# Optimization experiments

Hardware: AMD Instinct MI355X
Metric: run time of the kernel (lower is better)

Reference implementation:

```python
import jax, jax.numpy as jnp
import numpy as np

B, N, P, D = 16, 358, 72, 96
ND, H, K = 64, 4, 10
HL = H // 2
HG = H - HL
NH = 4  # temporal attention heads


def ln(x, g, b, eps=1e-5):
    m = x.mean(-1, keepdims=True)
    v = ((x - m) ** 2).mean(-1, keepdims=True)
    return (x - m) / jnp.sqrt(v + eps) * g + b


def topk_sparsify(adj, k):
    # row-wise top-k masking + renormalization, vectorized over all leading dims
    shp = adj.shape
    n = shp[-1]
    flat = adj.reshape(-1, shp[-2], n)
    M, R = flat.shape[0], flat.shape[1]
    _, idx = jax.lax.top_k(flat, k)  # (M,R,k)
    mask = jnp.zeros(flat.shape, flat.dtype).at[
        jnp.arange(M)[:, None, None], jnp.arange(R)[None, :, None], idx].set(1.0)
    sp = flat * mask
    sp = sp / (sp.sum(-1, keepdims=True) + 1e-8)
    return sp.reshape(shp)


def forward(patch_features, local_e1, local_e2, global_e1, global_e2, static_e2,
            temperature, pos_enc, wq, bq, wk, bk, wv, bv, wo, bo, tn_g, tn_b,
            de_w1, de_b1, de_g1, de_beta1, de_w2, de_b2, de_g2, de_beta2,
            gnn_w, gnn_b, gnn_g, gnn_beta, gf_w, gf_b,
            ee_w1, ee_b1, ee_g, ee_beta, ee_w2, ee_b2, ee_w3, ee_b3):
    # ---- static multi-head graphs (batched over heads instead of python loop) ----
    adj_l = jax.nn.relu(jnp.einsum('hnd,hdm->hnm', local_e1, local_e2))
    t_l = jnp.clip(temperature[:HL] * 2.0, 0.1, 5.0)
    adj_l = jax.nn.softmax(adj_l / t_l[:, None, None], axis=-1)
    adj_g = jax.nn.relu(jnp.einsum('hnd,hdm->hnm', global_e1, global_e2))
    t_g = jnp.clip(temperature[HL:] * 0.5, 0.1, 2.0)
    adj_g = jax.nn.softmax(adj_g / t_g[:, None, None], axis=-1)
    static_adjs = jnp.concatenate([adj_l, adj_g], axis=0)  # (H,N,N)

    # ---- dynamic graphs ----
    b, n, p, d = patch_features.shape
    pr = patch_features.reshape(b * n, p, d)
    x = pr + pos_enc[:, :p]
    hd = d // NH
    q = (x @ wq + bq).reshape(-1, p, NH, hd).transpose(0, 2, 1, 3)
    kk = (x @ wk + bk).reshape(-1, p, NH, hd).transpose(0, 2, 1, 3)
    v = (x @ wv + bv).reshape(-1, p, NH, hd).transpose(0, 2, 1, 3)
    att = jax.nn.softmax(jnp.einsum('bhqd,bhkd->bhqk', q, kk) / np.float32(np.sqrt(hd)), axis=-1)
    o = jnp.einsum('bhqk,bhkd->bhqd', att, v).transpose(0, 2, 1, 3).reshape(-1, p, d)
    attended = o @ wo + bo  # (BN,P,D)
    imp = jax.nn.softmax(attended.mean(-1), axis=1)  # (BN,P)
    node = (attended * imp[..., None]).sum(1) + pr.mean(1)
    node = ln(node, tn_g, tn_b).reshape(b, n, d)
    h1 = jax.nn.gelu(ln(node @ de_w1 + de_b1, de_g1, de_beta1), approximate=False)
    dyn = ln(h1 @ de_w2 + de_b2, de_g2, de_beta2)  # (B,N,ND)
    for i in range(2):  # 2 structurally distinct GNN layers, batched over B
        sim = jax.nn.softmax(jnp.einsum('bnd,bmd->bnm', dyn, dyn) / 0.2, axis=-1)
        agg = jnp.einsum('bnm,bmd->bnd', sim, dyn)
        out = jax.nn.gelu(ln(agg @ gnn_w[i] + gnn_b[i], gnn_g[i], gnn_beta[i]), approximate=False)
        dyn = out + dyn
    dsim = jax.nn.relu(jnp.einsum('bnd,hdm->bhnm', dyn, static_e2))
    t_d = jnp.clip(temperature, 0.1, 2.0)
    dynamic_adjs = jax.nn.softmax(dsim / t_d[None, :, None, None], axis=-1)  # (B,H,N,N)

    static_adjs = topk_sparsify(static_adjs, K)
    dynamic_adjs = topk_sparsify(dynamic_adjs, K)

    # ---- static/dynamic fusion ----
    node_f = patch_features.mean(2)  # (B,N,D)
    fw = jax.nn.sigmoid(node_f @ gf_w + gf_b)  # (B,N,H)
    w = jnp.transpose(fw, (0, 2, 1))[..., None]  # (B,H,N,1), broadcast over columns
    fused = (1.0 - w) * static_adjs[None] + w * dynamic_adjs  # (B,H,N,N)

    # ---- edge encoder over head dim ----
    mh = jnp.transpose(fused, (0, 2, 3, 1))  # (B,N,N,H)
    e = jax.nn.gelu(ln(mh @ ee_w1 + ee_b1, ee_g, ee_beta), approximate=False)
    e = jax.nn.gelu(e @ ee_w2 + ee_b2, approximate=False)
    e = (e @ ee_w3 + ee_b3)[..., 0]  # (B,N,N)
    final = jax.nn.sigmoid(e) * fused.mean(1)
    return final, static_adjs, dynamic_adjs


def setup_inputs() -> dict:
    key = jax.random.key(0)
    ks = jax.random.split(key, 20)
    r = lambda i, shape, s=0.05: jax.random.normal(ks[i], shape, dtype=jnp.float32) * s
    z = lambda shape: jnp.zeros(shape, jnp.float32)
    o = lambda shape: jnp.ones(shape, jnp.float32)
    return dict(
        patch_features=r(0, (B, N, P, D), 1.0),
        local_e1=r(1, (HL, N, ND // 2), 0.1),
        local_e2=r(2, (HL, ND // 2, N), 0.1),
        global_e1=r(3, (HG, N, ND), 0.1),
        global_e2=r(4, (HG, ND, N), 0.1),
        static_e2=r(5, (H, ND, N), 0.1),
        temperature=jnp.full((H,), 0.5, jnp.float32),
        pos_enc=r(6, (1, 72, D), 0.02),
        wq=r(7, (D, D)), bq=z((D,)),
        wk=r(8, (D, D)), bk=z((D,)),
        wv=r(9, (D, D)), bv=z((D,)),
        wo=r(10, (D, D)), bo=z((D,)),
        tn_g=o((D,)), tn_b=z((D,)),
        de_w1=r(11, (D, 2 * ND)), de_b1=z((2 * ND,)),
        de_g1=o((2 * ND,)), de_beta1=z((2 * ND,)),
        de_w2=r(12, (2 * ND, ND)), de_b2=z((ND,)),
        de_g2=o((ND,)), de_beta2=z((ND,)),
        gnn_w=r(13, (2, ND, ND)), gnn_b=z((2, ND)),
        gnn_g=o((2, ND)), gnn_beta=z((2, ND)),
        gf_w=r(14, (D, H)), gf_b=z((H,)),
        ee_w1=r(15, (H, 4 * H)), ee_b1=z((4 * H,)),
        ee_g=o((4 * H,)), ee_beta=z((4 * H,)),
        ee_w2=r(16, (4 * H, 2 * H)), ee_b2=z((2 * H,)),
        ee_w3=r(17, (2 * H, 1)), ee_b3=z((1,)),
    )


def reference(patch_features, local_e1, local_e2, global_e1, global_e2, static_e2,
              temperature, pos_enc, wq, bq, wk, bk, wv, bv, wo, bo, tn_g, tn_b,
              de_w1, de_b1, de_g1, de_beta1, de_w2, de_b2, de_g2, de_beta2,
              gnn_w, gnn_b, gnn_g, gnn_beta, gf_w, gf_b,
              ee_w1, ee_b1, ee_g, ee_beta, ee_w2, ee_b2, ee_w3, ee_b3):
    return forward(patch_features, local_e1, local_e2, global_e1, global_e2, static_e2,
                   temperature, pos_enc, wq, bq, wk, bk, wv, bv, wo, bo, tn_g, tn_b,
                   de_w1, de_b1, de_g1, de_beta1, de_w2, de_b2, de_g2, de_beta2,
                   gnn_w, gnn_b, gnn_g, gnn_beta, gf_w, gf_b,
                   ee_w1, ee_b1, ee_g, ee_beta, ee_w2, ee_b2, ee_w3, ee_b3)
```

## Files before the change

### kernel.cpp

```cpp
#include <hip/hip_runtime.h>
#include <hip/hip_bf16.h>

#define B_ 16
#define N_ 358
#define P_ 72
#define D_ 96
#define ND_ 64
#define H_ 4
#define NH_ 4
#define HD_ 24
#define K_ 10
#define BN_ (B_*N_)
#define NN_ (N_*N_)
#define RPW_ 6

__device__ __forceinline__ float gelu_f(float x){ return 0.5f*x*(1.0f+erff(x*0.7071067811865476f)); }
__device__ __forceinline__ float sigm_f(float x){ return 1.0f/(1.0f+expf(-x)); }

__global__ __launch_bounds__(256) void attn_kernel(
    const float* __restrict__ patch, const float* __restrict__ pos,
    const float* __restrict__ wq, const float* __restrict__ bq,
    const float* __restrict__ wk, const float* __restrict__ bk,
    const float* __restrict__ wv, const float* __restrict__ bv,
    const float* __restrict__ wo, const float* __restrict__ bo,
    const float* __restrict__ tng, const float* __restrict__ tnb,
    float* __restrict__ node_out, float* __restrict__ meanpr_out)
{
    __shared__ float smem[10656];
    __shared__ float rr[P_];
    __shared__ float nb[D_];
    __shared__ float st2[2];

    float* const xs  = smem;
    float* const qh  = smem;
    float* const kh  = smem + 1800;
    float* const vh  = smem + 3600;
    float* const att = smem + 5400;
    float* const ats = smem;

    const int tid = threadIdx.x;
    const int tc  = tid & 31;
    const int tr  = tid >> 5;
    const int rbase = tr * 9;
    const int bn  = blockIdx.x;
    const float* pr = patch + (size_t)bn * (P_*D_);

    float mpr = 0.f;
    if (tid < D_) {
        for (int p = 0; p < P_; ++p) mpr += pr[p*D_+tid];
        mpr *= (1.0f/P_);
        meanpr_out[(size_t)bn*D_ + tid] = mpr;
    }

    for (int e = tid; e < P_*D_; e += 256) {
        int row = e / D_, col = e - row*D_;
        xs[row*97 + col] = pr[e] + pos[e];
    }
    __syncthreads();

    float aq[3][9], ak[3][9], av[3][9];
    #pragma unroll
    for (int j = 0; j < 3; ++j) {
        const int c = tc + 32*j;
        const float vbq = bq[c], vbk = bk[c], vbv = bv[c];
        #pragma unroll
        for (int i = 0; i < 9; ++i) { aq[j][i]=vbq; ak[j][i]=vbk; av[j][i]=vbv; }
    }
    for (int k = 0; k < D_; ++k) {
        float xv[9];
        #pragma unroll
        for (int i = 0; i < 9; ++i) xv[i] = xs[(rbase+i)*97 + k];
        const float* wqp = wq + k*D_;
        const float* wkp = wk + k*D_;
        const float* wvp = wv + k*D_;
        float wqv[3], wkv[3], wvv[3];
        #pragma unroll
        for (int j = 0; j < 3; ++j) {
            const int c = tc + 32*j;
            wqv[j]=wqp[c]; wkv[j]=wkp[c]; wvv[j]=wvp[c];
        }
        #pragma unroll
        for (int j = 0; j < 3; ++j)
            #pragma unroll
            for (int i = 0; i < 9; ++i) {
                aq[j][i] += xv[i]*wqv[j];
                ak[j][i] += xv[i]*wkv[j];
                av[j][i] += xv[i]*wvv[j];
            }
    }
    __syncthreads();

    float ao[3][9];
    #pragma unroll
    for (int j = 0; j < 3; ++j) {
        const float vbo = bo[tc + 32*j];
        #pragma unroll
        for (int i = 0; i < 9; ++i) ao[j][i] = vbo;
    }

    const float rs = 0.20412414523193154f;
    for (int h = 0; h < NH_; ++h) {
        #pragma unroll
        for (int j = 0; j < 3; ++j) {
            const int c = tc + 32*j;
            const int dl = c - HD_*h;
            if ((unsigned)dl < (unsigned)HD_) {
                #pragma unroll
                for (int i = 0; i < 9; ++i) {
                    qh[(rbase+i)*25 + dl] = aq[j][i];
                    kh[(rbase+i)*25 + dl] = ak[j][i];
                    vh[(rbase+i)*25 + dl] = av[j][i];
                }
            }
        }
        __syncthreads();

        {
            float sc[3][9];
            #pragma unroll
            for (int jj = 0; jj < 3; ++jj)
                #pragma unroll
                for (int i = 0; i < 9; ++i) sc[jj][i] = 0.f;
            for (int d = 0; d < HD_; ++d) {
                float qv[9];
                #pragma unroll
                for (int i = 0; i < 9; ++i) qv[i] = qh[(rbase+i)*25 + d];
                float kv[3];
                #pragma unroll
                for (int jj = 0; jj < 3; ++jj) {
                    const int jn = tc + 32*jj;
                    kv[jj] = (jn < P_) ? kh[jn*25 + d] : 0.f;
                }
                #pragma unroll
                for (int jj = 0; jj < 3; ++jj)
                    #pragma unroll
                    for (int i = 0; i < 9; ++i) sc[jj][i] += qv[i]*kv[jj];
            }
            #pragma unroll
            for (int jj = 0; jj < 3; ++jj) {
                const int jn = tc + 32*jj;
                if (jn < P_) {
                    #pragma unroll
                    for (int i = 0; i < 9; ++i)
                        att[(rbase+i)*73 + jn] = sc[jj][i]*rs;
                }
            }
        }
        __syncthreads();

        if (tid < P_) {
            float* ar = att + tid*73;
            float mx = ar[0];
            for (int j = 1; j < P_; ++j) mx = fmaxf(mx, ar[j]);
            float sm = 0.f;
            for (int j = 0; j < P_; ++j) { float ev = expf(ar[j]-mx); ar[j]=ev; sm += ev; }
            float inv = 1.0f/sm;
            for (int j = 0; j < P_; ++j) ar[j] *= inv;
        }
        __syncthreads();

        if (tc < HD_) {
            float ov[9];
            #pragma unroll
            for (int i = 0; i < 9; ++i) ov[i] = 0.f;
            for (int j = 0; j < P_; ++j) {
                const float vv = vh[j*25 + tc];
                #pragma unroll
                for (int i = 0; i < 9; ++i) ov[i] += att[(rbase+i)*73 + j]*vv;
            }
            #pragma unroll
            for (int i = 0; i < 9; ++i) kh[(rbase+i)*25 + tc] = ov[i];
        }
        __syncthreads();

        for (int d = 0; d < HD_; ++d) {
            float ovv[9];
            #pragma unroll
            for (int i = 0; i < 9; ++i) ovv[i] = kh[(rbase+i)*25 + d];
            const float* wop = wo + (HD_*h + d)*D_;
            float wv3[3];
            #pragma unroll
            for (int j = 0; j < 3; ++j) wv3[j] = wop[tc + 32*j];
            #pragma unroll
            for (int j = 0; j < 3; ++j)
                #pragma unroll
                for (int i = 0; i < 9; ++i) ao[j][i] += ovv[i]*wv3[j];
        }
        __syncthreads();
    }

    #pragma unroll
    for (int j = 0; j < 3; ++j) {
        const int c = tc + 32*j;
        #pragma unroll
        for (int i = 0; i < 9; ++i) ats[(rbase+i)*97 + c] = ao[j][i];
    }
    __syncthreads();

    if (tid < P_) {
        const float* ar = ats + tid*97;
        float s = 0.f;
        for (int d = 0; d < D_; ++d) s += ar[d];
        rr[tid] = s*(1.0f/D_);
    }
    __syncthreads();
    if (tid == 0) {
        float mx = rr[0];
        for (int i=1;i<P_;++i) mx = fmaxf(mx, rr[i]);
        float sm=0.f;
        for (int i=0;i<P_;++i){ float ev=expf(rr[i]-mx); rr[i]=ev; sm+=ev; }
        float inv=1.0f/sm;
        for (int i=0;i<P_;++i) rr[i]*=inv;
    }
    __syncthreads();
    if (tid < D_) {
        float s = 0.f;
        for (int i=0;i<P_;++i) s += ats[i*97+tid]*rr[i];
        nb[tid] = s + mpr;
    }
    __syncthreads();
    if (tid == 0) {
        float m=0.f; for(int d=0;d<D_;++d) m+=nb[d]; m *= (1.0f/D_);
        float v=0.f; for(int d=0;d<D_;++d){ float df=nb[d]-m; v+=df*df; } v *= (1.0f/D_);
        st2[0]=m; st2[1]=rsqrtf(v+1e-5f);
    }
    __syncthreads();
    if (tid < D_) {
        float y = (nb[tid]-st2[0])*st2[1]*tng[tid] + tnb[tid];
        node_out[(size_t)bn*D_+tid] = y;
    }
}

__global__ __launch_bounds__(128) void enc1_kernel(
    const float* __restrict__ node, const float* __restrict__ w1, const float* __restrict__ b1,
    const float* __restrict__ g1, const float* __restrict__ be1, float* __restrict__ h1)
{
    __shared__ float nr[D_];
    __shared__ float buf[128];
    __shared__ float st2[2];
    const int tid = threadIdx.x; const int bn = blockIdx.x;
    if (tid < D_) nr[tid] = node[(size_t)bn*D_+tid];
    __syncthreads();
    float s = b1[tid];
    for (int c = 0; c < D_; ++c) s += nr[c]*w1[c*128+tid];
    buf[tid] = s;
    __syncthreads();
    if (tid == 0) {
        float m=0.f; for(int d=0;d<128;++d) m+=buf[d]; m *= (1.0f/128.0f);
        float v=0.f; for(int d=0;d<128;++d){ float df=buf[d]-m; v+=df*df; } v *= (1.0f/128.0f);
        st2[0]=m; st2[1]=rsqrtf(v+1e-5f);
    }
    __syncthreads();
    float y = (buf[tid]-st2[0])*st2[1]*g1[tid] + be1[tid];
    h1[(size_t)bn*128+tid] = gelu_f(y);
}

__global__ __launch_bounds__(64) void enc2_kernel(
    const float* __restrict__ h1, const float* __restrict__ w2, const float* __restrict__ b2,
    const float* __restrict__ g2, const float* __restrict__ be2, float* __restrict__ dyn)
{
    __shared__ float hr[128];
    __shared__ float buf[ND_];
    __shared__ float st2[2];
    const int tid = threadIdx.x; const int bn = blockIdx.x;
    hr[tid] = h1[(size_t)bn*128+tid];
    hr[tid+64] = h1[(size_t)bn*128+64+tid];
    __syncthreads();
    float s = b2[tid];
    for (int c = 0; c < 128; ++c) s += hr[c]*w2[c*ND_+tid];
    buf[tid] = s;
    __syncthreads();
    if (tid == 0) {
        float m=0.f; for(int d=0;d<ND_;++d) m+=buf[d]; m *= (1.0f/ND_);
        float v=0.f; for(int d=0;d<ND_;++d){ float df=buf[d]-m; v+=df*df; } v *= (1.0f/ND_);
        st2[0]=m; st2[1]=rsqrtf(v+1e-5f);
    }
    __syncthreads();
    dyn[(size_t)bn*ND_+tid] = (buf[tid]-st2[0])*st2[1]*g2[tid] + be2[tid];
}

__global__ __launch_bounds__(256) void gnn_kernel(
    const float* __restrict__ din, float* __restrict__ dout,
    const float* __restrict__ gw, const float* __restrict__ gb,
    const float* __restrict__ gg, const float* __restrict__ gbe, int layer)
{
    __shared__ float dq[ND_];
    __shared__ float prob[N_];
    __shared__ float red[256];
    __shared__ float aggp[4*ND_];
    __shared__ float buf[ND_];
    __shared__ float st2[2];
    const int tid = threadIdx.x; const int bn = blockIdx.x;
    const int b = bn / N_;
    const float* base = din + (size_t)b*N_*ND_;
    if (tid < ND_) dq[tid] = din[(size_t)bn*ND_+tid];
    __syncthreads();

    float lmax = -1e30f;
    for (int m = tid; m < N_; m += 256) {
        const float* rm = base + (size_t)m*ND_;
        float s = 0.f;
        for (int c = 0; c < ND_; ++c) s += dq[c]*rm[c];
        s *= 5.0f;
        prob[m] = s;
        lmax = fmaxf(lmax, s);
    }
    red[tid]=lmax; __syncthreads();
    for (int st=128; st>0; st>>=1){ if(tid<st) red[tid]=fmaxf(red[tid],red[tid+st]); __syncthreads(); }
    const float mx = red[0]; __syncthreads();
    float lsum = 0.f;
    for (int m=tid; m<N_; m+=256){ float ev=expf(prob[m]-mx); prob[m]=ev; lsum+=ev; }
    red[tid]=lsum; __syncthreads();
    for (int st=128; st>0; st>>=1){ if(tid<st) red[tid]+=red[tid+st]; __syncthreads(); }
    const float inv = 1.0f/red[0]; __syncthreads();
    for (int m=tid; m<N_; m+=256) prob[m]*=inv;
    __syncthreads();

    {
        const int part = tid >> 6, d = tid & 63;
        float s = 0.f;
        for (int m = part; m < N_; m += 4) s += prob[m]*base[(size_t)m*ND_+d];
        aggp[part*ND_+d] = s;
    }
    __syncthreads();
    if (tid < ND_)
        aggp[tid] = aggp[tid]+aggp[ND_+tid]+aggp[2*ND_+tid]+aggp[3*ND_+tid];
    __syncthreads();
    if (tid < ND_) {
        float t = gb[layer*ND_+tid];
        for (int c = 0; c < ND_; ++c) t += aggp[c]*gw[(layer*ND_+c)*ND_+tid];
        buf[tid] = t;
    }
    __syncthreads();
    if (tid == 0) {
        float m=0.f; for(int d=0;d<ND_;++d) m+=buf[d]; m *= (1.0f/ND_);
        float v=0.f; for(int d=0;d<ND_;++d){ float df=buf[d]-m; v+=df*df; } v *= (1.0f/ND_);
        st2[0]=m; st2[1]=rsqrtf(v+1e-5f);
    }
    __syncthreads();
    if (tid < ND_) {
        float y = (buf[tid]-st2[0])*st2[1]*gg[layer*ND_+tid] + gbe[layer*ND_+tid];
        dout[(size_t)bn*ND_+tid] = gelu_f(y) + dq[tid];
    }
}

__device__ __forceinline__ void wave_softmax_topk_store(
    float lv[RPW_], int lane, float* __restrict__ outrow)
{
    float mx = 0.f;
    #pragma unroll
    for (int j=0;j<RPW_;++j) mx = fmaxf(mx, lv[j]);
    #pragma unroll
    for (int s=1;s<64;s<<=1) mx = fmaxf(mx, __shfl_xor(mx, s));
    float sm = 0.f;
    #pragma unroll
    for (int j=0;j<RPW_;++j) {
        const int m = lane + 64*j;
        const float e = (m < N_) ? expf(lv[j]-mx) : 0.f;
        lv[j] = e; sm += e;
    }
    #pragma unroll
    for (int s=1;s<64;s<<=1) sm += __shfl_xor(sm, s);
    const float inv = 1.0f/sm;
    #pragma unroll
    for (int j=0;j<RPW_;++j) lv[j] *= inv;

    unsigned sel = 0u;
    float ksum = 0.f;
    for (int it = 0; it < K_; ++it) {
        float bv = -1.f; int bm = 0x7fffffff;
        #pragma unroll
        for (int j=0;j<RPW_;++j) {
            const int m = lane + 64*j;
            if (m < N_ && !((sel>>j)&1u) && lv[j] > bv) { bv = lv[j]; bm = m; }
        }
        #pragma unroll
        for (int s=1;s<64;s<<=1) {
            const float ov = __shfl_xor(bv, s);
            const int   om = __shfl_xor(bm, s);
            if (ov > bv || (ov == bv && om < bm)) { bv = ov; bm = om; }
        }
        ksum += bv;
        if ((bm & 63) == lane) sel |= 1u << (bm >> 6);
    }
    const float dn = 1.0f/(ksum + 1e-8f);
    #pragma unroll
    for (int j=0;j<RPW_;++j) {
        const int m = lane + 64*j;
        if (m < N_) outrow[m] = ((sel>>j)&1u) ? lv[j]*dn : 0.f;
    }
}

__global__ __launch_bounds__(256) void static_adj_kernel(
    const float* __restrict__ le1, const float* __restrict__ le2,
    const float* __restrict__ ge1, const float* __restrict__ ge2,
    const float* __restrict__ temp, float* __restrict__ outs)
{
    __shared__ float e1l[4][ND_];
    const int tid = threadIdx.x;
    const int wv = tid >> 6, lane = tid & 63;
    const int r = blockIdx.x*4 + wv;
    const int h = r / N_, n = r % N_;
    if (h < 2) { if (lane < 32) e1l[wv][lane] = le1[(h*N_+n)*32+lane]; }
    else       { e1l[wv][lane] = ge1[((h-2)*N_+n)*64+lane]; }
    __syncthreads();
    const float t = temp[h];
    const float tl = (h < 2) ? fminf(fmaxf(t*2.0f,0.1f),5.0f) : fminf(fmaxf(t*0.5f,0.1f),2.0f);
    const float invt = 1.0f/tl;
    float lv[RPW_];
    #pragma unroll
    for (int j=0;j<RPW_;++j) lv[j] = 0.f;
    if (h < 2) {
        for (int c = 0; c < 32; ++c) {
            const float dc = e1l[wv][c];
            const float* sr = le2 + (size_t)(h*32+c)*N_;
            #pragma unroll
            for (int j=0;j<RPW_;++j) {
                const int m = lane + 64*j;
                if (m < N_) lv[j] += dc*sr[m];
            }
        }
    } else {
        for (int c = 0; c < 64; ++c) {
            const float dc = e1l[wv][c];
            const float* sr = ge2 + (size_t)((h-2)*64+c)*N_;
            #pragma unroll
            for (int j=0;j<RPW_;++j) {
                const int m = lane + 64*j;
                if (m < N_) lv[j] += dc*sr[m];
            }
        }
    }
    #pragma unroll
    for (int j=0;j<RPW_;++j) lv[j] = fmaxf(lv[j],0.f)*invt;
    wave_softmax_topk_store(lv, lane, outs + (size_t)r*N_);
}

__global__ __launch_bounds__(256) void dyn_adj_kernel(
    const float* __restrict__ dyn, const float* __restrict__ se2,
    const float* __restrict__ temp, float* __restrict__ outd)
{
    __shared__ float dql[4][ND_];
    const int tid = threadIdx.x;
    const int wv = tid >> 6, lane = tid & 63;
    const int r = blockIdx.x*4 + wv;
    const int b = r / (H_*N_);
    const int rem = r % (H_*N_);
    const int h = rem / N_, n = rem % N_;
    dql[wv][lane] = dyn[((size_t)(b*N_+n))*ND_ + lane];
    __syncthreads();
    const float invt = 1.0f/fminf(fmaxf(temp[h],0.1f),2.0f);
    float lv[RPW_];
    #pragma unroll
    for (int j=0;j<RPW_;++j) lv[j] = 0.f;
    const float* sb = se2 + (size_t)h*ND_*N_;
    for (int c = 0; c < ND_; ++c) {
        const float dc = dql[wv][c];
        const float* sr = sb + (size_t)c*N_;
        #pragma unroll
        for (int j=0;j<RPW_;++j) {
            const int m = lane + 64*j;
            if (m < N_) lv[j] += dc*sr[m];
        }
    }
    #pragma unroll
    for (int j=0;j<RPW_;++j) lv[j] = fmaxf(lv[j],0.f)*invt;
    wave_softmax_topk_store(lv, lane, outd + ((size_t)(b*H_+h)*N_+n)*(size_t)N_);
}

__global__ __launch_bounds__(256) void fw_kernel(
    const float* __restrict__ meanpr, const float* __restrict__ gfw,
    const float* __restrict__ gfb, float* __restrict__ wf)
{
    const int gid = blockIdx.x*256 + threadIdx.x;
    if (gid >= BN_*H_) return;
    const int bn = gid >> 2, h = gid & 3;
    float s = gfb[h];
    const float* mp = meanpr + (size_t)bn*D_;
    for (int c=0;c<D_;++c) s += mp[c]*gfw[c*H_+h];
    wf[gid] = sigm_f(s);
}

__global__ __launch_bounds__(256) void edge_kernel(
    const float* __restrict__ staticf, const float* __restrict__ dynf,
    const float* __restrict__ wf,
    const float* __restrict__ ew1, const float* __restrict__ eb1,
    const float* __restrict__ eg,  const float* __restrict__ ebe,
    const float* __restrict__ ew2, const float* __restrict__ eb2,
    const float* __restrict__ ew3, const float* __restrict__ eb3,
    float* __restrict__ outf)
{
    __shared__ float w1s[64], w2s[128], b1s[16], gs[16], bes[16], b2s[8], w3s[8];
    __shared__ float b3v;
    const int tid = threadIdx.x;
    if (tid < 64)                 w1s[tid]     = ew1[tid];
    else if (tid < 192)           w2s[tid-64]  = ew2[tid-64];
    else if (tid < 208)           b1s[tid-192] = eb1[tid-192];
    else if (tid < 224)           gs[tid-208]  = eg[tid-208];
    else if (tid < 240)           bes[tid-224] = ebe[tid-224];
    else if (tid < 248)           b2s[tid-240] = eb2[tid-240];
    else                          w3s[tid-248] = ew3[tid-248];
    if (tid == 0) b3v = eb3[0];
    __syncthreads();

    const size_t gid = (size_t)blockIdx.x*256 + tid;
    if (gid >= (size_t)B_*NN_) return;
    const int m = (int)(gid % N_);
    const size_t t1 = gid / N_;
    const int n = (int)(t1 % N_);
    const int b = (int)(t1 / N_);

    const float* wrow = wf + ((size_t)(b*N_+n))*4;
    float mh[4]; float msum = 0.f;
    #pragma unroll
    for (int h=0; h<4; ++h) {
        float w  = wrow[h];
        float st = staticf[((size_t)(h*N_+n))*N_ + m];
        float da = dynf[(((size_t)(b*4+h))*N_+n)*(size_t)N_ + m];
        float f = (1.0f-w)*st + w*da;
        mh[h] = f; msum += f;
    }
    float e16[16]; float mean = 0.f;
    #pragma unroll
    for (int j=0;j<16;++j) {
        float s = b1s[j];
        #pragma unroll
        for (int h=0;h<4;++h) s += mh[h]*w1s[h*16+j];
        e16[j] = s; mean += s;
    }
    mean *= (1.0f/16.0f);
    float var = 0.f;
    #pragma unroll
    for (int j=0;j<16;++j){ float df=e16[j]-mean; var += df*df; }
    var *= (1.0f/16.0f);
    const float rinv = rsqrtf(var + 1e-5f);
    #pragma unroll
    for (int j=0;j<16;++j) e16[j] = gelu_f((e16[j]-mean)*rinv*gs[j] + bes[j]);
    float e8[8];
    #pragma unroll
    for (int o=0;o<8;++o) {
        float s = b2s[o];
        #pragma unroll
        for (int j=0;j<16;++j) s += e16[j]*w2s[j*8+o];
        e8[o] = gelu_f(s);
    }
    float e = b3v;
    #pragma unroll
    for (int o=0;o<8;++o) e += e8[o]*w3s[o];
    outf[gid] = sigm_f(e) * (msum*0.25f);
}

extern "C" void kernel_launch(void* const* d_in, const int* in_sizes, int n_in,
                              void* d_out, int out_size, void* d_ws, size_t ws_size,
                              hipStream_t stream)
{
    const float* patch = (const float*)d_in[0];
    const float* le1   = (const float*)d_in[1];
    const float* le2   = (const float*)d_in[2];
    const float* ge1   = (const float*)d_in[3];
    const float* ge2   = (const float*)d_in[4];
    const float* se2   = (const float*)d_in[5];
    const float* temp  = (const float*)d_in[6];
    const float* pos   = (const float*)d_in[7];
    const float* wq    = (const float*)d_in[8];
    const float* bq    = (const float*)d_in[9];
    const float* wk    = (const float*)d_in[10];
    const float* bk    = (const float*)d_in[11];
    const float* wv    = (const float*)d_in[12];
    const float* bv    = (const float*)d_in[13];
    const float* wo    = (const float*)d_in[14];
    const float* bo    = (const float*)d_in[15];
    const float* tng   = (const float*)d_in[16];
    const float* tnb   = (const float*)d_in[17];
    const float* dw1   = (const float*)d_in[18];
    const float* db1   = (const float*)d_in[19];
    const float* dg1   = (const float*)d_in[20];
    const float* dbe1  = (const float*)d_in[21];
    const float* dw2   = (const float*)d_in[22];
    const float* db2   = (const float*)d_in[23];
    const float* dg2   = (const float*)d_in[24];
    const float* dbe2  = (const float*)d_in[25];
    const float* gw    = (const float*)d_in[26];
    const float* gb    = (const float*)d_in[27];
    const float* gg    = (const float*)d_in[28];
    const float* gbe   = (const float*)d_in[29];
    const float* gfw   = (const float*)d_in[30];
    const float* gfb   = (const float*)d_in[31];
    const float* ew1   = (const float*)d_in[32];
    const float* eb1   = (const float*)d_in[33];
    const float* eg    = (const float*)d_in[34];
    const float* ebe   = (const float*)d_in[35];
    const float* ew2   = (const float*)d_in[36];
    const float* eb2   = (const float*)d_in[37];
    const float* ew3   = (const float*)d_in[38];
    const float* eb3   = (const float*)d_in[39];
    (void)in_sizes; (void)n_in; (void)out_size; (void)ws_size;

    float* ws      = (float*)d_ws;
    float* meanpr  = ws;
    float* node    = meanpr + (size_t)BN_*D_;
    float* h1      = node   + (size_t)BN_*D_;
    float* dyn0    = h1     + (size_t)BN_*128;
    float* dyn1    = node;
    float* wfuse   = h1;

    float* out        = (float*)d_out;
    float* out_final  = out;
    float* out_static = out + (size_t)B_*NN_;
    float* out_dyn    = out_static + (size_t)H_*NN_;

    attn_kernel<<<BN_, 256, 0, stream>>>(patch,pos,wq,bq,wk,bk,wv,bv,wo,bo,tng,tnb,node,meanpr);
    enc1_kernel<<<BN_, 128, 0, stream>>>(node,dw1,db1,dg1,dbe1,h1);
    enc2_kernel<<<BN_, 64,  0, stream>>>(h1,dw2,db2,dg2,dbe2,dyn0);
    gnn_kernel<<<BN_, 256, 0, stream>>>(dyn0,dyn1,gw,gb,gg,gbe,0);
    gnn_kernel<<<BN_, 256, 0, stream>>>(dyn1,dyn0,gw,gb,gg,gbe,1);
    static_adj_kernel<<<H_*N_/4, 256, 0, stream>>>(le1,le2,ge1,ge2,temp,out_static);
    dyn_adj_kernel<<<B_*H_*N_/4, 256, 0, stream>>>(dyn0,se2,temp,out_dyn);
    fw_kernel<<<(BN_*H_+255)/256, 256, 0, stream>>>(meanpr,gfw,gfb,wfuse);
    edge_kernel<<<((size_t)B_*NN_+255)/256, 256, 0, stream>>>(
        out_static,out_dyn,wfuse,ew1,eb1,eg,ebe,ew2,eb2,ew3,eb3,out_final);
}
```

Before: 2.866 ms.

## Split temporal attention into per-head QKV blocks and separate output-projection kernel

The monolithic attention kernel, where one block handled all four heads serially, is replaced by two kernels. The first launches one block per (node, head) and computes only that head's Q/K/V projection, scores, softmax and PV. The second does the output projection, importance pooling and layer norm. Chunks of nodes are processed in a loop, with the output buffer as scratch. This gives four times more blocks and shorter serial chains per block, at the cost of staging the full x tile redundantly per head, idling 8 of 32 lanes per row, and an extra global round trip plus more launches.

```diff
diff --git a/kernel.cpp b/kernel.cpp
--- a/kernel.cpp
+++ b/kernel.cpp
@@ -13,43 +13,38 @@
 #define BN_ (B_*N_)
 #define NN_ (N_*N_)
 #define RPW_ 6
+#define CHUNK_ 1432
 
 __device__ __forceinline__ float gelu_f(float x){ return 0.5f*x*(1.0f+erff(x*0.7071067811865476f)); }
 __device__ __forceinline__ float sigm_f(float x){ return 1.0f/(1.0f+expf(-x)); }
 
-__global__ __launch_bounds__(256) void attn_kernel(
+__global__ __launch_bounds__(256) void attn_qkv_kernel(
     const float* __restrict__ patch, const float* __restrict__ pos,
     const float* __restrict__ wq, const float* __restrict__ bq,
     const float* __restrict__ wk, const float* __restrict__ bk,
     const float* __restrict__ wv, const float* __restrict__ bv,
-    const float* __restrict__ wo, const float* __restrict__ bo,
-    const float* __restrict__ tng, const float* __restrict__ tnb,
-    float* __restrict__ node_out, float* __restrict__ meanpr_out)
+    int bn0, float* __restrict__ obuf, float* __restrict__ meanpr_out)
 {
     __shared__ float smem[10656];
-    __shared__ float rr[P_];
-    __shared__ float nb[D_];
-    __shared__ float st2[2];
-
     float* const xs  = smem;
     float* const qh  = smem;
     float* const kh  = smem + 1800;
     float* const vh  = smem + 3600;
     float* const att = smem + 5400;
-    float* const ats = smem;
 
     const int tid = threadIdx.x;
     const int tc  = tid & 31;
     const int tr  = tid >> 5;
     const int rbase = tr * 9;
-    const int bn  = blockIdx.x;
+    const int bnl = blockIdx.x >> 2;
+    const int h   = blockIdx.x & 3;
+    const int bn  = bn0 + bnl;
     const float* pr = patch + (size_t)bn * (P_*D_);
 
-    float mpr = 0.f;
-    if (tid < D_) {
-        for (int p = 0; p < P_; ++p) mpr += pr[p*D_+tid];
-        mpr *= (1.0f/P_);
-        meanpr_out[(size_t)bn*D_ + tid] = mpr;
+    if (h == 0 && tid < D_) {
+        float s = 0.f;
+        for (int p = 0; p < P_; ++p) s += pr[p*D_+tid];
+        meanpr_out[(size_t)bn*D_ + tid] = s * (1.0f/P_);
     }
 
     for (int e = tid; e < P_*D_; e += 256) {
@@ -58,147 +53,155 @@
     }
     __syncthreads();
 
-    float aq[3][9], ak[3][9], av[3][9];
+    float aq[9], ak[9], av[9];
+    const int col = h*HD_ + tc;
+    if (tc < HD_) {
+        const float vbq = bq[col], vbk = bk[col], vbv = bv[col];
+        #pragma unroll
+        for (int i = 0; i < 9; ++i) { aq[i]=vbq; ak[i]=vbk; av[i]=vbv; }
+        for (int k = 0; k < D_; ++k) {
+            float xv[9];
+            #pragma unroll
+            for (int i = 0; i < 9; ++i) xv[i] = xs[(rbase+i)*97 + k];
+            const float wqv = wq[k*D_+col];
+            const float wkv = wk[k*D_+col];
+            const float wvv = wv[k*D_+col];
+            #pragma unroll
+            for (int i = 0; i < 9; ++i) {
+                aq[i] += xv[i]*wqv;
+                ak[i] += xv[i]*wkv;
+                av[i] += xv[i]*wvv;
+            }
+        }
+    }
+    __syncthreads();
+
+    if (tc < HD_) {
+        #pragma unroll
+        for (int i = 0; i < 9; ++i) {
+            qh[(rbase+i)*25 + tc] = aq[i];
+            kh[(rbase+i)*25 + tc] = ak[i];
+            vh[(rbase+i)*25 + tc] = av[i];
+        }
+    }
+    __syncthreads();
+
+    const float rs = 0.20412414523193154f;
+    {
+        float sc[3][9];
+        #pragma unroll
+        for (int jj = 0; jj < 3; ++jj)
+            #pragma unroll
+            for (int i = 0; i < 9; ++i) sc[jj][i] = 0.f;
+        for (int d = 0; d < HD_; ++d) {
+            float qv[9];
+            #pragma unroll
+            for (int i = 0; i < 9; ++i) qv[i] = qh[(rbase+i)*25 + d];
+            float kv[3];
+            #pragma unroll
+            for (int jj = 0; jj < 3; ++jj) {
+                const int jn = tc + 32*jj;
+                kv[jj] = (jn < P_) ? kh[jn*25 + d] : 0.f;
+            }
+            #pragma unroll
+            for (int jj = 0; jj < 3; ++jj)
+                #pragma unroll
+                for (int i = 0; i < 9; ++i) sc[jj][i] += qv[i]*kv[jj];
+        }
+        #pragma unroll
+        for (int jj = 0; jj < 3; ++jj) {
+            const int jn = tc + 32*jj;
+            if (jn < P_) {
+                #pragma unroll
+                for (int i = 0; i < 9; ++i)
+                    att[(rbase+i)*73 + jn] = sc[jj][i]*rs;
+            }
+        }
+    }
+    __syncthreads();
+
+    if (tid < P_) {
+        float* ar = att + tid*73;
+        float mx = ar[0];
+        for (int j = 1; j < P_; ++j) mx = fmaxf(mx, ar[j]);
+        float sm = 0.f;
+        for (int j = 0; j < P_; ++j) { float ev = expf(ar[j]-mx); ar[j]=ev; sm += ev; }
+        float inv = 1.0f/sm;
+        for (int j = 0; j < P_; ++j) ar[j] *= inv;
+    }
+    __syncthreads();
+
+    if (tc < HD_) {
+        float ov[9];
+        #pragma unroll
+        for (int i = 0; i < 9; ++i) ov[i] = 0.f;
+        for (int j = 0; j < P_; ++j) {
+            const float vv = vh[j*25 + tc];
+            #pragma unroll
+            for (int i = 0; i < 9; ++i) ov[i] += att[(rbase+i)*73 + j]*vv;
+        }
+        #pragma unroll
+        for (int i = 0; i < 9; ++i)
+            obuf[((size_t)bnl*P_ + rbase+i)*D_ + col] = ov[i];
+    }
+}
+
+__global__ __launch_bounds__(256) void attn_oproj_kernel(
+    const float* __restrict__ obuf, const float* __restrict__ wo,
+    const float* __restrict__ bo, const float* __restrict__ tng,
+    const float* __restrict__ tnb, const float* __restrict__ meanpr,
+    int bn0, float* __restrict__ node_out)
+{
+    __shared__ float xs[P_*97];
+    __shared__ float rr[P_];
+    __shared__ float nb[D_];
+    __shared__ float st2[2];
+
+    const int tid = threadIdx.x;
+    const int tc  = tid & 31;
+    const int tr  = tid >> 5;
+    const int rbase = tr * 9;
+    const int bnl = blockIdx.x;
+    const int bn  = bn0 + bnl;
+
+    const float* orow = obuf + (size_t)bnl*(P_*D_);
+    for (int e = tid; e < P_*D_; e += 256) {
+        int row = e / D_, col = e - row*D_;
+        xs[row*97 + col] = orow[e];
+    }
+    __syncthreads();
+
+    float ao[3][9];
+    #pragma unroll
+    for (int j = 0; j < 3; ++j) {
+        const float vbo = bo[tc + 32*j];
+        #pragma unroll
+        for (int i = 0; i < 9; ++i) ao[j][i] = vbo;
+    }
+    for (int k = 0; k < D_; ++k) {
+        float xv[9];
+        #pragma unroll
+        for (int i = 0; i < 9; ++i) xv[i] = xs[(rbase+i)*97 + k];
+        const float* wop = wo + k*D_;
+        float wv3[3];
+        #pragma unroll
+        for (int j = 0; j < 3; ++j) wv3[j] = wop[tc + 32*j];
+        #pragma unroll
+        for (int j = 0; j < 3; ++j)
+            #pragma unroll
+            for (int i = 0; i < 9; ++i) ao[j][i] += xv[i]*wv3[j];
+    }
+    __syncthreads();
     #pragma unroll
     for (int j = 0; j < 3; ++j) {
         const int c = tc + 32*j;
-        const float vbq = bq[c], vbk = bk[c], vbv = bv[c];
-        #pragma unroll
-        for (int i = 0; i < 9; ++i) { aq[j][i]=vbq; ak[j][i]=vbk; av[j][i]=vbv; }
-    }
-    for (int k = 0; k < D_; ++k) {
-        float xv[9];
-        #pragma unroll
-        for (int i = 0; i < 9; ++i) xv[i] = xs[(rbase+i)*97 + k];
-        const float* wqp = wq + k*D_;
-        const float* wkp = wk + k*D_;
-        const float* wvp = wv + k*D_;
-        float wqv[3], wkv[3], wvv[3];
-        #pragma unroll
-        for (int j = 0; j < 3; ++j) {
-            const int c = tc + 32*j;
-            wqv[j]=wqp[c]; wkv[j]=wkp[c]; wvv[j]=wvp[c];
-        }
-        #pragma unroll
-        for (int j = 0; j < 3; ++j)
-            #pragma unroll
-            for (int i = 0; i < 9; ++i) {
-                aq[j][i] += xv[i]*wqv[j];
-                ak[j][i] += xv[i]*wkv[j];
-                av[j][i] += xv[i]*wvv[j];
-            }
-    }
-    __syncthreads();
-
-    float ao[3][9];
-    #pragma unroll
-    for (int j = 0; j < 3; ++j) {
-        const float vbo = bo[tc + 32*j];
-        #pragma unroll
-        for (int i = 0; i < 9; ++i) ao[j][i] = vbo;
-    }
-
-    const float rs = 0.20412414523193154f;
-    for (int h = 0; h < NH_; ++h) {
-        #pragma unroll
-        for (int j = 0; j < 3; ++j) {
-            const int c = tc + 32*j;
-            const int dl = c - HD_*h;
-            if ((unsigned)dl < (unsigned)HD_) {
-                #pragma unroll
-                for (int i = 0; i < 9; ++i) {
-                    qh[(rbase+i)*25 + dl] = aq[j][i];
-                    kh[(rbase+i)*25 + dl] = ak[j][i];
-                    vh[(rbase+i)*25 + dl] = av[j][i];
-                }
-            }
-        }
-        __syncthreads();
-
-        {
-            float sc[3][9];
-            #pragma unroll
-            for (int jj = 0; jj < 3; ++jj)
-                #pragma unroll
-                for (int i = 0; i < 9; ++i) sc[jj][i] = 0.f;
-            for (int d = 0; d < HD_; ++d) {
-                float qv[9];
-                #pragma unroll
-                for (int i = 0; i < 9; ++i) qv[i] = qh[(rbase+i)*25 + d];
-                float kv[3];
-                #pragma unroll
-                for (int jj = 0; jj < 3; ++jj) {
-                    const int jn = tc + 32*jj;
-                    kv[jj] = (jn < P_) ? kh[jn*25 + d] : 0.f;
-                }
-                #pragma unroll
-                for (int jj = 0; jj < 3; ++jj)
-                    #pragma unroll
-                    for (int i = 0; i < 9; ++i) sc[jj][i] += qv[i]*kv[jj];
-            }
-            #pragma unroll
-            for (int jj = 0; jj < 3; ++jj) {
-                const int jn = tc + 32*jj;
-                if (jn < P_) {
-                    #pragma unroll
-                    for (int i = 0; i < 9; ++i)
-                        att[(rbase+i)*73 + jn] = sc[jj][i]*rs;
-                }
-            }
-        }
-        __syncthreads();
-
-        if (tid < P_) {
-            float* ar = att + tid*73;
-            float mx = ar[0];
-            for (int j = 1; j < P_; ++j) mx = fmaxf(mx, ar[j]);
-            float sm = 0.f;
-            for (int j = 0; j < P_; ++j) { float ev = expf(ar[j]-mx); ar[j]=ev; sm += ev; }
-            float inv = 1.0f/sm;
-            for (int j = 0; j < P_; ++j) ar[j] *= inv;
-        }
-        __syncthreads();
-
-        if (tc < HD_) {
-            float ov[9];
-            #pragma unroll
-            for (int i = 0; i < 9; ++i) ov[i] = 0.f;
-            for (int j = 0; j < P_; ++j) {
-                const float vv = vh[j*25 + tc];
-                #pragma unroll
-                for (int i = 0; i < 9; ++i) ov[i] += att[(rbase+i)*73 + j]*vv;
-            }
-            #pragma unroll
-            for (int i = 0; i < 9; ++i) kh[(rbase+i)*25 + tc] = ov[i];
-        }
-        __syncthreads();
-
-        for (int d = 0; d < HD_; ++d) {
-            float ovv[9];
-            #pragma unroll
-            for (int i = 0; i < 9; ++i) ovv[i] = kh[(rbase+i)*25 + d];
-            const float* wop = wo + (HD_*h + d)*D_;
-            float wv3[3];
-            #pragma unroll
-            for (int j = 0; j < 3; ++j) wv3[j] = wop[tc + 32*j];
-            #pragma unroll
-            for (int j = 0; j < 3; ++j)
-                #pragma unroll
-                for (int i = 0; i < 9; ++i) ao[j][i] += ovv[i]*wv3[j];
-        }
-        __syncthreads();
-    }
-
-    #pragma unroll
-    for (int j = 0; j < 3; ++j) {
-        const int c = tc + 32*j;
-        #pragma unroll
-        for (int i = 0; i < 9; ++i) ats[(rbase+i)*97 + c] = ao[j][i];
+        #pragma unroll
+        for (int i = 0; i < 9; ++i) xs[(rbase+i)*97 + c] = ao[j][i];
     }
     __syncthreads();
 
     if (tid < P_) {
-        const float* ar = ats + tid*97;
+        const float* ar = xs + tid*97;
         float s = 0.f;
         for (int d = 0; d < D_; ++d) s += ar[d];
         rr[tid] = s*(1.0f/D_);
@@ -215,8 +218,8 @@
     __syncthreads();
     if (tid < D_) {
         float s = 0.f;
-        for (int i=0;i<P_;++i) s += ats[i*97+tid]*rr[i];
-        nb[tid] = s + mpr;
+        for (int i=0;i<P_;++i) s += xs[i*97+tid]*rr[i];
+        nb[tid] = s + meanpr[(size_t)bn*D_+tid];
     }
     __syncthreads();
     if (tid == 0) {
@@ -609,7 +612,15 @@
     float* out_static = out + (size_t)B_*NN_;
     float* out_dyn    = out_static + (size_t)H_*NN_;
 
-    attn_kernel<<<BN_, 256, 0, stream>>>(patch,pos,wq,bq,wk,bk,wv,bv,wo,bo,tng,tnb,node,meanpr);
+    float* obuf = out;
+
+    for (int c = 0; c < BN_/CHUNK_; ++c) {
+        const int bn0 = c*CHUNK_;
+        attn_qkv_kernel<<<CHUNK_*4, 256, 0, stream>>>(
+            patch,pos,wq,bq,wk,bk,wv,bv,bn0,obuf,meanpr);
+        attn_oproj_kernel<<<CHUNK_, 256, 0, stream>>>(
+            obuf,wo,bo,tng,tnb,meanpr,bn0,node);
+    }
     enc1_kernel<<<BN_, 128, 0, stream>>>(node,dw1,db1,dg1,dbe1,h1);
     enc2_kernel<<<BN_, 64,  0, stream>>>(h1,dw2,db2,dg2,dbe2,dyn0);
     gnn_kernel<<<BN_, 256, 0, stream>>>(dyn0,dyn1,gw,gb,gg,gbe,0);
```

Result: slower. 3.114 ms (+8.6%).
